# Performance work log

Measured on AMD Instinct MI355X. Metric: run time of the kernel, lower is better.

Reference implementation:

```python
import jax, jax.numpy as jnp
import numpy as np

DIM = 768
TIME_DIM = 768
NUM_HEADS = 12
NUM_PATCHES = 784
GRID = 28  # sqrt(NUM_PATCHES)
REL_MAX = 2 * GRID - 1  # 55


def _rel_pos_indices():
    # Faithful to the torch buffer: relative_position_index = (dh + g-1) + (dw + g-1)
    coords = np.stack(np.meshgrid(np.arange(GRID), np.arange(GRID), indexing='ij'))  # [2,g,g]
    cf = coords.reshape(2, -1)  # [2,N]
    rel = cf[:, :, None] - cf[:, None, :]  # [2,N,N]
    rel = rel.transpose(1, 2, 0)
    rel[:, :, 0] += GRID - 1
    rel[:, :, 1] += GRID - 1
    idx = rel.sum(-1)  # [N,N], values in [0, 2*(2g-2)]
    # forward then splits this summed index (as written in the source):
    ih = idx // REL_MAX
    iw = idx % REL_MAX
    return jnp.asarray(ih, jnp.int32), jnp.asarray(iw, jnp.int32)


def setup_inputs() -> dict:
    key = jax.random.key(0)
    ks = jax.random.split(key, 16)
    B = 8
    s = 0.02
    inp = {
        'x_s': jax.random.normal(ks[0], (B, NUM_PATCHES, DIM), jnp.float32),
        'x_t': jax.random.normal(ks[1], (B, TIME_DIM), jnp.float32),
        'Wqs': jax.random.normal(ks[2], (DIM, DIM), jnp.float32) * s,
        'Wqt': jax.random.normal(ks[3], (TIME_DIM, DIM), jnp.float32) * s,
        'Wks': jax.random.normal(ks[4], (DIM, DIM), jnp.float32) * s,
        'Wkt': jax.random.normal(ks[5], (TIME_DIM, DIM), jnp.float32) * s,
        'Wvs': jax.random.normal(ks[6], (DIM, DIM), jnp.float32) * s,
        'Wvt': jax.random.normal(ks[7], (TIME_DIM, DIM), jnp.float32) * s,
        'rpb_table': jax.random.normal(ks[8], (REL_MAX, REL_MAX, NUM_HEADS), jnp.float32) * s,
        'proj_w': jax.random.normal(ks[9], (DIM, DIM), jnp.float32) * s,
        'proj_b': jnp.zeros((DIM,), jnp.float32),
    }
    return inp


def reference(x_s, x_t, Wqs, Wqt, Wks, Wkt, Wvs, Wvt, rpb_table, proj_w, proj_b):
    B, N, D = x_s.shape
    H = NUM_HEADS
    hd = D // H
    scale = hd ** -0.5

    # time-embed fused QKV: q = x_s @ Wqs + x_t @ Wqt (broadcast over tokens)
    q = x_s @ Wqs + (x_t @ Wqt)[:, None, :]
    k = x_s @ Wks + (x_t @ Wkt)[:, None, :]
    v = x_s @ Wvs + (x_t @ Wvt)[:, None, :]

    q = q.reshape(B, N, H, hd).transpose(0, 2, 1, 3)  # [B,H,N,hd]
    k = k.reshape(B, N, H, hd).transpose(0, 2, 1, 3)
    v = v.reshape(B, N, H, hd).transpose(0, 2, 1, 3)

    attn = jnp.einsum('bhnd,bhmd->bhnm', q, k) * scale  # [B,H,N,N]

    ih, iw = _rel_pos_indices()  # [N,N] each
    bias = rpb_table[ih, iw]  # [N,N,H]
    attn = attn + bias.transpose(2, 0, 1)[None]  # [1,H,N,N]

    attn = jax.nn.softmax(attn, axis=-1)
    x = jnp.einsum('bhnm,bhmd->bhnd', attn, v)
    x = x.transpose(0, 2, 1, 3).reshape(B, N, D)
    return x @ proj_w + proj_b
```

## Files before the change

### kernel.cpp

```cpp
#include <hip/hip_runtime.h>
#include <hip/hip_bf16.h>
#include <stdint.h>

#define DIM 768
#define NP  784
#define NH  12
#define HD  64
#define BATCH 8
#define MROWS (BATCH*NP)
#define MPAD 832
#define NCHUNK 32
#define KCH 24
#define L2E 1.4426950408889634f

using bf16x8 = __attribute__((ext_vector_type(8))) short;
using bf16x4 = __attribute__((ext_vector_type(4))) short;
using f32x4  = __attribute__((ext_vector_type(4))) float;

__device__ __forceinline__ short f2bf(float f) {
  union { float f; uint32_t u; } c; c.f = f;
  uint32_t u = c.u;
  u += 0x7FFFu + ((u >> 16) & 1u);
  return (short)(u >> 16);
}

__device__ __forceinline__ short bfr(float x) {
  union { __hip_bfloat16 b; short s; } u;
  u.b = __float2bfloat16(x);
  return u.s;
}

__device__ __forceinline__ void gld_lds16(const void* g, void* l) {
  __builtin_amdgcn_global_load_lds((const __attribute__((address_space(1))) uint32_t*)g,
                                   (__attribute__((address_space(3))) uint32_t*)l,
                                   16, 0, 0);
}

__global__ __launch_bounds__(256) void prep_kernel(const float* __restrict__ x_s,
                                                   const float* __restrict__ x_t,
                                                   const float* __restrict__ Wqs,
                                                   const float* __restrict__ Wqt,
                                                   const float* __restrict__ Wks,
                                                   const float* __restrict__ Wkt,
                                                   const float* __restrict__ Wvs,
                                                   const float* __restrict__ Wvt,
                                                   const float* __restrict__ pw,
                                                   short* __restrict__ Xb,
                                                   short* __restrict__ Wt,
                                                   float* __restrict__ part) {
  __shared__ float tile[32][33];
  __shared__ float xs[BATCH][KCH];
  const int bid = blockIdx.x, tid = threadIdx.x;

  if (bid < 2352) {
    const int i = bid * 256 + tid;
    const float4* s = (const float4*)x_s;
    float4 a = s[2*i], b = s[2*i+1];
    bf16x8 o;
    o[0]=f2bf(a.x); o[1]=f2bf(a.y); o[2]=f2bf(a.z); o[3]=f2bf(a.w);
    o[4]=f2bf(b.x); o[5]=f2bf(b.y); o[6]=f2bf(b.z); o[7]=f2bf(b.w);
    ((bf16x8*)Xb)[i] = o;
  } else if (bid < 4656) {
    int r = bid - 2352;
    const int z = r / 576; r -= z * 576;
    const int bxx = r % 24, byy = r / 24;
    const float* src = (z==0) ? Wqs : (z==1) ? Wks : (z==2) ? Wvs : pw;
    short* d = Wt + (size_t)z * DIM * DIM;
    const int n0 = bxx*32, k0 = byy*32;
    const int tx = tid & 31, ty = tid >> 5;
#pragma unroll
    for (int i=0;i<4;i++) tile[ty+i*8][tx] = src[(size_t)(k0+ty+i*8)*DIM + n0+tx];
    __syncthreads();
#pragma unroll
    for (int i=0;i<4;i++) d[(size_t)(n0+ty+i*8)*DIM + k0+tx] = f2bf(tile[tx][ty+i*8]);
  } else {
    int r = bid - 4656;
    const int z = r >> 5, kc = r & 31;
    const float* w = (z==0) ? Wqt : (z==1) ? Wkt : Wvt;
    const int d = tid;
    if (tid < BATCH*KCH)
      xs[tid / KCH][tid % KCH] = x_t[(size_t)(tid / KCH)*DIM + kc*KCH + tid % KCH];
    __syncthreads();
    float a0[BATCH] = {}, a1[BATCH] = {}, a2[BATCH] = {};
#pragma unroll 4
    for (int k = 0; k < KCH; ++k) {
      const float* wr = w + (size_t)(kc*KCH + k)*DIM + d;
      float w0 = wr[0], w1 = wr[256], w2 = wr[512];
#pragma unroll
      for (int b = 0; b < BATCH; ++b) {
        float xv = xs[b][k];
        a0[b] += xv*w0; a1[b] += xv*w1; a2[b] += xv*w2;
      }
    }
#pragma unroll
    for (int b = 0; b < BATCH; ++b) {
      float* p = part + (((size_t)z*NCHUNK + kc)*BATCH + b)*DIM + d;
      p[0] = a0[b]; p[256] = a1[b]; p[512] = a2[b];
    }
  }
}

__global__ __launch_bounds__(256) void tvec2_kernel(const float* __restrict__ part,
                                                    float* __restrict__ t) {
  const int i = blockIdx.x*256 + threadIdx.x;
  if (i >= 3*BATCH*DIM) return;
  const int z = i / (BATCH*DIM), rem = i % (BATCH*DIM);
  float s = 0.f;
#pragma unroll 8
  for (int c = 0; c < NCHUNK; ++c)
    s += part[((size_t)z*NCHUNK + c)*BATCH*DIM + rem];
  t[i] = s;
}

__global__ __launch_bounds__(512, 1) void qkv256_kernel(const short* __restrict__ A,
                                                        const short* __restrict__ Wt,
                                                        const float* __restrict__ aux,
                                                        short* __restrict__ outq,
                                                        short* __restrict__ outk,
                                                        short* __restrict__ outv) {
  __shared__ short As0[256*64];
  __shared__ short As1[256*64];
  __shared__ short Bs0[256*64];
  __shared__ short Bs1[256*64];
  const int bx = blockIdx.x, by = blockIdx.y;
  const int z = bx / 3;
  const int n0z = (bx - z*3) * 256;
  const short* Bz = Wt + (size_t)z * DIM * DIM;
  const int m0 = by * 256;
  const int tid = threadIdx.x, w = tid >> 6, lane = tid & 63;
  const int wr = w >> 2, wc = w & 3, ln15 = lane & 15, lg = lane >> 4;

  const int lr8 = lane >> 3, c8e = (lane & 7) * 8;
  const int swe = c8e ^ (lr8 << 3);
  const short* aS = A  + (size_t)(m0  + w*8 + lr8) * DIM + swe;
  const short* bS = Bz + (size_t)(n0z + w*8 + lr8) * DIM + swe;

#define STG2(DA, DB, TT) { \
    char* da_ = (char*)(DA) + w*1024; \
    char* db_ = (char*)(DB) + w*1024; \
    const int kk_ = (TT)*64; \
    gld_lds16(aS + (size_t)0*64*DIM + kk_, da_ + 0*8192); \
    gld_lds16(bS + (size_t)0*64*DIM + kk_, db_ + 0*8192); \
    gld_lds16(aS + (size_t)1*64*DIM + kk_, da_ + 1*8192); \
    gld_lds16(bS + (size_t)1*64*DIM + kk_, db_ + 1*8192); \
    gld_lds16(aS + (size_t)2*64*DIM + kk_, da_ + 2*8192); \
    gld_lds16(bS + (size_t)2*64*DIM + kk_, db_ + 2*8192); \
    gld_lds16(aS + (size_t)3*64*DIM + kk_, da_ + 3*8192); \
    gld_lds16(bS + (size_t)3*64*DIM + kk_, db_ + 3*8192); }

#define QBODY(AB, BB) { \
    _Pragma("unroll") \
    for (int ks = 0; ks < 2; ++ks) { \
      bf16x8 bfv[4]; \
      _Pragma("unroll") \
      for (int ni = 0; ni < 4; ++ni) { \
        const int row_ = wc*64 + ni*16 + ln15; \
        bfv[ni] = *(const bf16x8*)&(BB)[row_*64 + ((ks*32 + lg*8) ^ ((row_ & 7) << 3))]; \
      } \
      _Pragma("unroll") \
      for (int mi = 0; mi < 8; ++mi) { \
        const int row_ = wr*128 + mi*16 + ln15; \
        bf16x8 afv = *(const bf16x8*)&(AB)[row_*64 + ((ks*32 + lg*8) ^ ((row_ & 7) << 3))]; \
        _Pragma("unroll") \
        for (int ni = 0; ni < 4; ++ni) \
          acc[mi][ni] = __builtin_amdgcn_mfma_f32_16x16x32_bf16(afv, bfv[ni], acc[mi][ni], 0,0,0); \
      } \
    } }

  f32x4 acc[8][4] = {};

  STG2(As0, Bs0, 0)
  STG2(As1, Bs1, 1)

  for (int tt = 0; tt < 5; ++tt) {
    const int t2 = tt*2;
    asm volatile("s_waitcnt vmcnt(8)" ::: "memory");
    __builtin_amdgcn_s_barrier();
    QBODY(As0, Bs0)
    __builtin_amdgcn_s_barrier();
    STG2(As0, Bs0, t2+2)
    asm volatile("s_waitcnt vmcnt(8)" ::: "memory");
    __builtin_amdgcn_s_barrier();
    QBODY(As1, Bs1)
    __builtin_amdgcn_s_barrier();
    STG2(As1, Bs1, t2+3)
  }
  asm volatile("s_waitcnt vmcnt(8)" ::: "memory");
  __builtin_amdgcn_s_barrier();
  QBODY(As0, Bs0)
  __builtin_amdgcn_s_barrier();
  asm volatile("s_waitcnt vmcnt(0)" ::: "memory");
  __builtin_amdgcn_s_barrier();
  QBODY(As1, Bs1)

  const float scl = 0.125f * L2E;
#pragma unroll
  for (int ai = 0; ai < 8; ++ai) {
    const int rb = m0 + wr*128 + (ai>>2)*64 + (ai&3)*16 + lg*4;
    if (z == 2) {
      if (rb < MROWS) {
        const int bb = rb / NP;
        const int m  = rb - bb*NP;
        const float* tv = aux + ((size_t)2*BATCH + bb) * DIM;
#pragma unroll
        for (int ni = 0; ni < 4; ++ni) {
          const int col = n0z + wc*64 + ni*16 + ln15;
          const int h = col >> 6, d = col & 63;
          const float tb = tv[col];
          bf16x4 ov;
          ov[0] = f2bf(acc[ai][ni][0] + tb);
          ov[1] = f2bf(acc[ai][ni][1] + tb);
          ov[2] = f2bf(acc[ai][ni][2] + tb);
          ov[3] = f2bf(acc[ai][ni][3] + tb);
          *(bf16x4*)&outv[((size_t)(bb*NH + h)*HD + d)*MPAD + m] = ov;
        }
      }
    } else {
#pragma unroll
      for (int j = 0; j < 4; ++j) {
        const int r = rb + j;
        if (r < MROWS) {
          const int bb = r / NP;
          const int m  = r - bb*NP;
          const float* tv = aux + ((size_t)z*BATCH + bb) * DIM;
#pragma unroll
          for (int ni = 0; ni < 4; ++ni) {
            const int col = n0z + wc*64 + ni*16 + ln15;
            if (z == 0) {
              outq[(size_t)r*DIM + col] = f2bf((acc[ai][ni][j] + tv[col]) * scl);
            } else {
              const int h = col >> 6, d = col & 63;
              outk[((size_t)(bb*NH + h)*MPAD + m)*HD + d] = f2bf(acc[ai][ni][j] + tv[col]);
            }
          }
        }
      }
    }
  }
#undef STG2
#undef QBODY
}

template<int MODE>
__global__ __launch_bounds__(256) void gemm_kernel(const short* __restrict__ A,
                                                   const short* __restrict__ Bw,
                                                   const float* __restrict__ aux,
                                                   float* __restrict__ outf) {
  __shared__ short As[128*32];
  __shared__ short Bs[128*32];
  const int bx = blockIdx.x, by = blockIdx.y;
  const short* Bz = Bw;
  const int tid = threadIdx.x, w = tid>>6, lane = tid&63;
  const int wr = w>>1, wc = w&1, ln15 = lane&15, lg = lane>>4;
  const int m0 = by*128, n0 = bx*128;

  f32x4 acc[4][4] = {};

  for (int kt=0; kt<24; ++kt) {
    const int k0 = kt*32;
    __syncthreads();
#pragma unroll
    for (int i=0;i<2;i++) {
      const int inst = w*2 + i;
      const int off  = inst*1024 + lane*16;
      const int row  = off >> 6;
      const int ce   = (off & 63) >> 1;
      gld_lds16(A  + (size_t)(m0+row)*DIM + k0 + ce, (char*)As + (size_t)inst*1024);
      gld_lds16(Bz + (size_t)(n0+row)*DIM + k0 + ce, (char*)Bs + (size_t)inst*1024);
    }
    __syncthreads();
    bf16x8 af[4], bfr_[4];
#pragma unroll
    for (int mi=0;mi<4;mi++) af[mi]   = *(const bf16x8*)&As[(wr*64+mi*16+ln15)*32 + lg*8];
#pragma unroll
    for (int ni=0;ni<4;ni++) bfr_[ni] = *(const bf16x8*)&Bs[(wc*64+ni*16+ln15)*32 + lg*8];
#pragma unroll
    for (int mi=0;mi<4;mi++)
#pragma unroll
      for (int ni=0;ni<4;ni++)
        acc[mi][ni] = __builtin_amdgcn_mfma_f32_16x16x32_bf16(af[mi], bfr_[ni], acc[mi][ni], 0,0,0);
  }

#pragma unroll
  for (int mi=0;mi<4;mi++)
#pragma unroll
    for (int j=0;j<4;j++) {
      const int r = m0 + wr*64 + mi*16 + lg*4 + j;
#pragma unroll
      for (int ni=0;ni<4;ni++) {
        const int gcol = n0 + wc*64 + ni*16 + ln15;
        outf[(size_t)r*DIM + gcol] = acc[mi][ni][j] + aux[gcol];
      }
    }
}

__global__ __launch_bounds__(256, 3) void attn7_kernel(const short* __restrict__ Qb,
                                                       const short* __restrict__ Kt,
                                                       const short* __restrict__ Vt,
                                                       const float* __restrict__ rpb,
                                                       short* __restrict__ Ob) {
  __shared__ short kt[2][4096];
  __shared__ short vt[2][4096];
  __shared__ float4 bias4[112];
  const int hw = blockIdx.x;
  const int lgid = (hw & 7) * 84 + (hw >> 3);
  const int qt = lgid % 7;
  const int bh = lgid / 7;
  const int h = bh % NH, b = bh / NH;
  const int q0 = qt*128, tid = threadIdx.x, w = tid >> 6, lane = tid & 63;
  const int ln15 = lane & 15, lg = lane >> 4;

  if (tid < 112) {
    float4 v;
#pragma unroll
    for (int j = 0; j < 4; ++j) {
      const int i = tid - j - 2;
      float bv = 0.f;
      if (i >= 0 && i < 109)
        bv = rpb[(i/55)*(55*NH) + (i%55)*NH + h] * L2E;
      ((float*)&v)[j] = bv;
    }
    bias4[tid] = v;
  }

  const bool actA = (q0 + w*16) < NP;
  const bool actB = (q0 + 64 + w*16) < NP;
  const int qA = q0 + w*16 + ln15;
  const int qB = qA + 64;
  bf16x8 qfA0 = {}, qfA1 = {}, qfB0 = {}, qfB1 = {};
  if (actA) {
    const short* qp = Qb + ((size_t)(b*NP) + qA)*DIM + h*HD + lg*8;
    qfA0 = *(const bf16x8*)qp;
    qfA1 = *(const bf16x8*)(qp + 32);
  }
  if (actB) {
    const short* qp = Qb + ((size_t)(b*NP) + qB)*DIM + h*HD + lg*8;
    qfB0 = *(const bf16x8*)qp;
    qfB1 = *(const bf16x8*)(qp + 32);
  }
  const int qs56A = qA/28 + qA%28 + 56;
  const int qs56B = qB/28 + qB%28 + 56;

  const int lr = lane >> 3, lc = lane & 7;
  const int swe = (lc ^ lr) << 3;
  const size_t bhs = (size_t)bh;
  const short* kp0 = Kt + (bhs*MPAD + (size_t)(w*16 + lr))*HD + swe;
  const short* kp1 = kp0 + 8*HD;
  const short* vp0 = Vt + (bhs*HD + (size_t)(w*16 + lr))*MPAD + swe;
  const short* vp1 = vp0 + 8*MPAD;

#define STAGE4(BUF) { \
    gld_lds16(kp0, (char*)kt[BUF] + w*2048); \
    gld_lds16(kp1, (char*)kt[BUF] + w*2048 + 1024); \
    gld_lds16(vp0, (char*)vt[BUF] + w*2048); \
    gld_lds16(vp1, (char*)vt[BUF] + w*2048 + 1024); \
    kp0 += 64*HD; kp1 += 64*HD; vp0 += 64; vp1 += 64; }

  float lA = 0.f, lB = 0.f;
  f32x4 oA0={}, oA1={}, oA2={}, oA3={};
  f32x4 oB0={}, oB1={}, oB2={}, oB3={};

  STAGE4(0)

  for (int t = 0; t < 13; ++t) {
    const int cur = t & 1;
    const int m0 = t * 64;
    __syncthreads();
    if (t < 12) STAGE4(cur^1)
    if (actA || actB) {
      const char* kb = (const char*)kt[cur];
      const int sw = (ln15 & 7) << 4;
      f32x4 sA[4], sB[4];
#pragma unroll
      for (int mc = 0; mc < 4; ++mc) {
        const int rb = (mc*16 + ln15) * 128;
        bf16x8 kf0 = *(const bf16x8*)(kb + rb + ((lg*16) ^ sw));
        bf16x8 kf1 = *(const bf16x8*)(kb + rb + ((lg*16 + 64) ^ sw));
        f32x4 a = {};
        a = __builtin_amdgcn_mfma_f32_16x16x32_bf16(kf0, qfA0, a, 0,0,0);
        a = __builtin_amdgcn_mfma_f32_16x16x32_bf16(kf1, qfA1, a, 0,0,0);
        sA[mc] = a;
        f32x4 c = {};
        c = __builtin_amdgcn_mfma_f32_16x16x32_bf16(kf0, qfB0, c, 0,0,0);
        c = __builtin_amdgcn_mfma_f32_16x16x32_bf16(kf1, qfB1, c, 0,0,0);
        sB[mc] = c;
      }
#pragma unroll
      for (int mc = 0; mc < 4; ++mc) {
        const int mb = m0 + mc*16 + lg*4;
        const int a28 = (mb * 2341) >> 16;
        const int rel = 27*a28 - mb;
        const float4 bA = bias4[qs56A + rel];
        const float4 bB = bias4[qs56B + rel];
        sA[mc][0] += bA.x; sA[mc][1] += bA.y; sA[mc][2] += bA.z; sA[mc][3] += bA.w;
        sB[mc][0] += bB.x; sB[mc][1] += bB.y; sB[mc][2] += bB.z; sB[mc][3] += bB.w;
      }
      if (m0 + 64 > NP) {
#pragma unroll
        for (int mc = 0; mc < 4; ++mc)
#pragma unroll
          for (int j = 0; j < 4; ++j)
            if (m0 + mc*16 + lg*4 + j >= NP) { sA[mc][j] = -1e30f; sB[mc][j] = -1e30f; }
      }
      float tsA = 0.f, tsB = 0.f;
      bf16x4 pbA[4], pbB[4];
#pragma unroll
      for (int mc = 0; mc < 4; ++mc) {
        float a0 = exp2f(sA[mc][0]), a1 = exp2f(sA[mc][1]);
        float a2 = exp2f(sA[mc][2]), a3 = exp2f(sA[mc][3]);
        float b0 = exp2f(sB[mc][0]), b1 = exp2f(sB[mc][1]);
        float b2 = exp2f(sB[mc][2]), b3 = exp2f(sB[mc][3]);
        tsA += (a0+a1)+(a2+a3);
        tsB += (b0+b1)+(b2+b3);
        pbA[mc][0]=bfr(a0); pbA[mc][1]=bfr(a1); pbA[mc][2]=bfr(a2); pbA[mc][3]=bfr(a3);
        pbB[mc][0]=bfr(b0); pbB[mc][1]=bfr(b1); pbB[mc][2]=bfr(b2); pbB[mc][3]=bfr(b3);
      }
      lA += tsA; lB += tsB;
      const char* vb = (const char*)vt[cur];
#pragma unroll
      for (int mc = 0; mc < 4; ++mc) {
        const int ib = (mc*32 + lg*8) ^ sw;
        bf16x4 vf0 = *(const bf16x4*)(vb + (0*16+ln15)*128 + ib);
        bf16x4 vf1 = *(const bf16x4*)(vb + (1*16+ln15)*128 + ib);
        bf16x4 vf2 = *(const bf16x4*)(vb + (2*16+ln15)*128 + ib);
        bf16x4 vf3 = *(const bf16x4*)(vb + (3*16+ln15)*128 + ib);
        oA0 = __builtin_amdgcn_mfma_f32_16x16x16bf16_1k(vf0, pbA[mc], oA0, 0,0,0);
        oA1 = __builtin_amdgcn_mfma_f32_16x16x16bf16_1k(vf1, pbA[mc], oA1, 0,0,0);
        oA2 = __builtin_amdgcn_mfma_f32_16x16x16bf16_1k(vf2, pbA[mc], oA2, 0,0,0);
        oA3 = __builtin_amdgcn_mfma_f32_16x16x16bf16_1k(vf3, pbA[mc], oA3, 0,0,0);
        oB0 = __builtin_amdgcn_mfma_f32_16x16x16bf16_1k(vf0, pbB[mc], oB0, 0,0,0);
        oB1 = __builtin_amdgcn_mfma_f32_16x16x16bf16_1k(vf1, pbB[mc], oB1, 0,0,0);
        oB2 = __builtin_amdgcn_mfma_f32_16x16x16bf16_1k(vf2, pbB[mc], oB2, 0,0,0);
        oB3 = __builtin_amdgcn_mfma_f32_16x16x16bf16_1k(vf3, pbB[mc], oB3, 0,0,0);
      }
    }
  }
#undef STAGE4

  if (actA) {
    float l = lA;
    l += __shfl_xor(l, 16);
    l += __shfl_xor(l, 32);
    const float inv = 1.0f / l;
    short* op = Ob + ((size_t)(b*NP) + qA)*DIM + h*HD + lg*4;
    bf16x4 ov;
    ov[0]=bfr(oA0[0]*inv); ov[1]=bfr(oA0[1]*inv); ov[2]=bfr(oA0[2]*inv); ov[3]=bfr(oA0[3]*inv);
    *(bf16x4*)(op + 0*16) = ov;
    ov[0]=bfr(oA1[0]*inv); ov[1]=bfr(oA1[1]*inv); ov[2]=bfr(oA1[2]*inv); ov[3]=bfr(oA1[3]*inv);
    *(bf16x4*)(op + 1*16) = ov;
    ov[0]=bfr(oA2[0]*inv); ov[1]=bfr(oA2[1]*inv); ov[2]=bfr(oA2[2]*inv); ov[3]=bfr(oA2[3]*inv);
    *(bf16x4*)(op + 2*16) = ov;
    ov[0]=bfr(oA3[0]*inv); ov[1]=bfr(oA3[1]*inv); ov[2]=bfr(oA3[2]*inv); ov[3]=bfr(oA3[3]*inv);
    *(bf16x4*)(op + 3*16) = ov;
  }
  if (actB) {
    float l = lB;
    l += __shfl_xor(l, 16);
    l += __shfl_xor(l, 32);
    const float inv = 1.0f / l;
    short* op = Ob + ((size_t)(b*NP) + qB)*DIM + h*HD + lg*4;
    bf16x4 ov;
    ov[0]=bfr(oB0[0]*inv); ov[1]=bfr(oB0[1]*inv); ov[2]=bfr(oB0[2]*inv); ov[3]=bfr(oB0[3]*inv);
    *(bf16x4*)(op + 0*16) = ov;
    ov[0]=bfr(oB1[0]*inv); ov[1]=bfr(oB1[1]*inv); ov[2]=bfr(oB1[2]*inv); ov[3]=bfr(oB1[3]*inv);
    *(bf16x4*)(op + 1*16) = ov;
    ov[0]=bfr(oB2[0]*inv); ov[1]=bfr(oB2[1]*inv); ov[2]=bfr(oB2[2]*inv); ov[3]=bfr(oB2[3]*inv);
    *(bf16x4*)(op + 2*16) = ov;
    ov[0]=bfr(oB3[0]*inv); ov[1]=bfr(oB3[1]*inv); ov[2]=bfr(oB3[2]*inv); ov[3]=bfr(oB3[3]*inv);
    *(bf16x4*)(op + 3*16) = ov;
  }
}

extern "C" void kernel_launch(void* const* d_in, const int* in_sizes, int n_in,
                              void* d_out, int out_size, void* d_ws, size_t ws_size,
                              hipStream_t stream) {
  const float* x_s = (const float*)d_in[0];
  const float* x_t = (const float*)d_in[1];
  const float* Wqs = (const float*)d_in[2];
  const float* Wqt = (const float*)d_in[3];
  const float* Wks = (const float*)d_in[4];
  const float* Wkt = (const float*)d_in[5];
  const float* Wvs = (const float*)d_in[6];
  const float* Wvt = (const float*)d_in[7];
  const float* rpb = (const float*)d_in[8];
  const float* pw  = (const float*)d_in[9];
  const float* pb  = (const float*)d_in[10];
  float* out = (float*)d_out;

  char* ws = (char*)d_ws;
  size_t off = 0;
  float* t_part = (float*)(ws + off); off += (size_t)3*NCHUNK*BATCH*DIM*4;
  float* t_vec  = (float*)(ws + off); off += (size_t)3*BATCH*DIM*4;
  short* Wt     = (short*)(ws + off); off += (size_t)4*DIM*DIM*2;
  short* Qb     = (short*)(ws + off); off += (size_t)MROWS*DIM*2;
  short* Ob     = (short*)(ws + off); off += (size_t)MROWS*DIM*2;
  short* Xb     = (short*)(ws + off); off += (size_t)(MROWS+256)*DIM*2;
  short* Kt     = (short*)(ws + off); off += (size_t)BATCH*NH*MPAD*HD*2;
  short* Vt     = (short*)(ws + off); off += (size_t)BATCH*NH*MPAD*HD*2;

  prep_kernel<<<4752, 256, 0, stream>>>(x_s, x_t, Wqs, Wqt, Wks, Wkt, Wvs, Wvt, pw,
                                        Xb, Wt, t_part);
  tvec2_kernel<<<72, 256, 0, stream>>>(t_part, t_vec);
  qkv256_kernel<<<dim3(9,25), 512, 0, stream>>>(Xb, Wt, t_vec, Qb, Kt, Vt);
  attn7_kernel<<<672, 256, 0, stream>>>(Qb, Kt, Vt, rpb, Ob);
  gemm_kernel<1><<<dim3(6,49,1), 256, 0, stream>>>(Ob, Wt + (size_t)3*DIM*DIM, pb, out);
}
```

Measured before the change: 126.0 us.

## Replace double-buffered direct-to-LDS loads with register-staged single LDS buffer

The attention kernel stops using async global-to-LDS loads into two LDS buffers. It now prefetches the next K/V tile into registers during compute and writes it to a single swizzled LDS buffer between two barriers. Halving LDS use lets occupancy rise from 3 to 4 blocks per CU. The cost is an extra barrier per iteration, more register pressure, and the tile load being exposed at each LDS write.

New measurement: 156.6 us. +24.3%, slower.

```diff
diff --git a/kernel.cpp b/kernel.cpp
--- a/kernel.cpp
+++ b/kernel.cpp
@@ -294,13 +294,13 @@
     }
 }
 
-__global__ __launch_bounds__(256, 3) void attn7_kernel(const short* __restrict__ Qb,
+__global__ __launch_bounds__(256, 4) void attn8_kernel(const short* __restrict__ Qb,
                                                        const short* __restrict__ Kt,
                                                        const short* __restrict__ Vt,
                                                        const float* __restrict__ rpb,
                                                        short* __restrict__ Ob) {
-  __shared__ short kt[2][4096];
-  __shared__ short vt[2][4096];
+  __shared__ short kt[64*64];
+  __shared__ short vt[64*64];
   __shared__ float4 bias4[112];
   const int hw = blockIdx.x;
   const int lgid = (hw & 7) * 84 + (hw >> 3);
@@ -342,33 +342,38 @@
   const int qs56B = qB/28 + qB%28 + 56;
 
   const int lr = lane >> 3, lc = lane & 7;
-  const int swe = (lc ^ lr) << 3;
   const size_t bhs = (size_t)bh;
-  const short* kp0 = Kt + (bhs*MPAD + (size_t)(w*16 + lr))*HD + swe;
-  const short* kp1 = kp0 + 8*HD;
-  const short* vp0 = Vt + (bhs*HD + (size_t)(w*16 + lr))*MPAD + swe;
-  const short* vp1 = vp0 + 8*MPAD;
-
-#define STAGE4(BUF) { \
-    gld_lds16(kp0, (char*)kt[BUF] + w*2048); \
-    gld_lds16(kp1, (char*)kt[BUF] + w*2048 + 1024); \
-    gld_lds16(vp0, (char*)vt[BUF] + w*2048); \
-    gld_lds16(vp1, (char*)vt[BUF] + w*2048 + 1024); \
-    kp0 += 64*HD; kp1 += 64*HD; vp0 += 64; vp1 += 64; }
+  const short* kg0 = Kt + (bhs*MPAD + (size_t)(w*16 + lr))*HD + lc*8;
+  const short* kg1 = kg0 + 8*HD;
+  const short* vg0 = Vt + (bhs*HD + (size_t)(w*16 + lr))*MPAD + lc*8;
+  const short* vg1 = vg0 + 8*MPAD;
+  const int swb = (lc*16) ^ (lr << 4);
+  char* kw0 = (char*)kt + (w*16 + lr)*128 + swb;
+  char* kw1 = kw0 + 8*128;
+  char* vw0 = (char*)vt + (w*16 + lr)*128 + swb;
+  char* vw1 = vw0 + 8*128;
+
+  int4 kr0, kr1, vr0, vr1;
+  kr0 = *(const int4*)kg0; kr1 = *(const int4*)kg1;
+  vr0 = *(const int4*)vg0; vr1 = *(const int4*)vg1;
+  kg0 += 64*HD; kg1 += 64*HD; vg0 += 64; vg1 += 64;
+  *(int4*)kw0 = kr0; *(int4*)kw1 = kr1;
+  *(int4*)vw0 = vr0; *(int4*)vw1 = vr1;
+  __syncthreads();
 
   float lA = 0.f, lB = 0.f;
   f32x4 oA0={}, oA1={}, oA2={}, oA3={};
   f32x4 oB0={}, oB1={}, oB2={}, oB3={};
 
-  STAGE4(0)
-
   for (int t = 0; t < 13; ++t) {
-    const int cur = t & 1;
     const int m0 = t * 64;
-    __syncthreads();
-    if (t < 12) STAGE4(cur^1)
+    if (t < 12) {
+      kr0 = *(const int4*)kg0; kr1 = *(const int4*)kg1;
+      vr0 = *(const int4*)vg0; vr1 = *(const int4*)vg1;
+      kg0 += 64*HD; kg1 += 64*HD; vg0 += 64; vg1 += 64;
+    }
     if (actA || actB) {
-      const char* kb = (const char*)kt[cur];
+      const char* kb = (const char*)kt;
       const int sw = (ln15 & 7) << 4;
       f32x4 sA[4], sB[4];
 #pragma unroll
@@ -416,7 +421,7 @@
         pbB[mc][0]=bfr(b0); pbB[mc][1]=bfr(b1); pbB[mc][2]=bfr(b2); pbB[mc][3]=bfr(b3);
       }
       lA += tsA; lB += tsB;
-      const char* vb = (const char*)vt[cur];
+      const char* vb = (const char*)vt;
 #pragma unroll
       for (int mc = 0; mc < 4; ++mc) {
         const int ib = (mc*32 + lg*8) ^ sw;
@@ -434,8 +439,13 @@
         oB3 = __builtin_amdgcn_mfma_f32_16x16x16bf16_1k(vf3, pbB[mc], oB3, 0,0,0);
       }
     }
-  }
-#undef STAGE4
+    __syncthreads();
+    if (t < 12) {
+      *(int4*)kw0 = kr0; *(int4*)kw1 = kr1;
+      *(int4*)vw0 = vr0; *(int4*)vw1 = vr1;
+    }
+    __syncthreads();
+  }
 
   if (actA) {
     float l = lA;
@@ -502,6 +512,6 @@
                                         Xb, Wt, t_part);
   tvec2_kernel<<<72, 256, 0, stream>>>(t_part, t_vec);
   qkv256_kernel<<<dim3(9,25), 512, 0, stream>>>(Xb, Wt, t_vec, Qb, Kt, Vt);
-  attn7_kernel<<<672, 256, 0, stream>>>(Qb, Kt, Vt, rpb, Ob);
+  attn8_kernel<<<672, 256, 0, stream>>>(Qb, Kt, Vt, rpb, Ob);
   gemm_kernel<1><<<dim3(6,49,1), 256, 0, stream>>>(Ob, Wt + (size_t)3*DIM*DIM, pb, out);
 }
```
